# Performance work log

Hardware: AMD Instinct MI355X
Metric: run time of the kernel (lower is better)

## Reference

```python
import jax, jax.numpy as jnp
import numpy as np

IN_DIMS = [3, 16, 16]
OUT_DIMS = [16, 16, 3]
GRID_SIZE = 8
SPLINE_ORDER = 3
GRID_RANGE = (-1.0, 1.0)
K = GRID_SIZE + SPLINE_ORDER  # number of B-spline basis functions = 11

# extended knot grid, identical for every feature (as in standard KAN layers)
_h = (GRID_RANGE[1] - GRID_RANGE[0]) / GRID_SIZE
GRID_NP = np.arange(-SPLINE_ORDER, GRID_SIZE + SPLINE_ORDER + 1, dtype=np.float32) * _h + GRID_RANGE[0]

# per-layer parameter slice boundaries: [coef, univariate_weight, residual_weight] per layer
_sizes = [0]
for di, do in zip(IN_DIMS, OUT_DIMS):
    _sizes.extend([di * do * K, di * do, di * do])
PARAM_IDX = np.cumsum(_sizes)
KAN_PARAMS_NUM = int(PARAM_IDX[-1])  # 4576


def bspline_basis(x, grid):
    """Cox-de Boor recursion. x: [...,], grid: [G]. Returns [..., K]."""
    x = x[..., None]
    b = ((x >= grid[:-1]) & (x < grid[1:])).astype(x.dtype)
    for p in range(1, SPLINE_ORDER + 1):
        left = (x - grid[:-(p + 1)]) / (grid[p:-1] - grid[:-(p + 1)]) * b[..., :-1]
        right = (grid[p + 1:] - x) / (grid[p + 1:] - grid[1:-p]) * b[..., 1:]
        b = left + right
    return b  # [..., GRID_SIZE + SPLINE_ORDER]


def setup_inputs() -> dict:
    key = jax.random.key(0)
    k1, k2, k3, k4 = jax.random.split(key, 4)
    B, C, H, W = 8, 3, 224, 224
    x = jax.random.uniform(k1, (B, C, H, W), dtype=jnp.float32)  # in grid range
    features = jax.random.normal(k2, (B, 1000), dtype=jnp.float32)  # resnet18 output stand-in
    fc_w = jax.random.normal(k3, (KAN_PARAMS_NUM, 1000), dtype=jnp.float32) * 0.02
    fc_b = jax.random.normal(k4, (KAN_PARAMS_NUM,), dtype=jnp.float32) * 0.02
    return {"x": x, "features": features, "fc_w": fc_w, "fc_b": fc_b}


def reference(x, features, fc_w, fc_b):
    B, C, H, W = x.shape
    # hypernetwork head: per-sample flat KAN parameter vector [B, P]
    w = features @ fc_w.T + fc_b
    # image -> per-pixel tokens [B, T, C]
    y = jnp.transpose(x, (0, 2, 3, 1)).reshape(B, H * W, C)
    grid = jnp.asarray(GRID_NP, dtype=x.dtype)
    for n, (di, do) in enumerate(zip(IN_DIMS, OUT_DIMS)):
        i0, i1, i2, i3 = PARAM_IDX[3 * n: 3 * n + 4]
        coef = w[:, i0:i1].reshape(B, di, do, K)       # spline coefficients
        uw = w[:, i1:i2].reshape(B, di, do)            # univariate (spline) weight
        rw = w[:, i2:i3].reshape(B, di, do)            # residual (silu) weight
        basis = bspline_basis(y, grid)                 # [B, T, di, K]
        spline = jnp.einsum('btik,biok->bto', basis, coef * uw[..., None])
        base = jnp.einsum('bti,bio->bto', jax.nn.silu(y), rw)
        y = spline + base                              # [B, T, do]
    out = y.reshape(B, H, W, -1)
    return jnp.transpose(out, (0, 3, 1, 2))
```

## Files before the change

### kernel.cpp

```cpp
#include <hip/hip_runtime.h>

#define HW   50176
#define NPAR 4576

typedef _Float16 half8 __attribute__((ext_vector_type(8)));
typedef __fp16 fp16x2 __attribute__((ext_vector_type(2)));
typedef __attribute__((ext_vector_type(4))) float f32x4;
typedef __attribute__((ext_vector_type(4))) int int4v;

__device__ __forceinline__ unsigned short f2h(float f) {
    union { _Float16 h; unsigned short u; } c; c.h = (_Float16)f; return c.u;
}
__device__ __forceinline__ float h2f(unsigned short u) {
    union { _Float16 h; unsigned short u; } c; c.u = u; return (float)c.h;
}
__device__ __forceinline__ int pkrtz(float lo, float hi) {
    union { fp16x2 h; int i; } c;
    c.h = __builtin_amdgcn_cvt_pkrtz(lo, hi);
    return c.i;
}

__global__ __launch_bounds__(256) void gemm_w(const float* __restrict__ feats,
                                              const float* __restrict__ fcw,
                                              const float* __restrict__ fcb,
                                              float* __restrict__ wout) {
    __shared__ float red[4][64][4];
    int tid = threadIdx.x, lane = tid & 63, wave = tid >> 6;
    int nn = lane & 15, quad = lane >> 4;
    int n = blockIdx.x * 16 + nn;
    const float* brow = fcw + (size_t)n * 1000;
    const float* arow = feats + nn * 1000;

    f32x4 acc = {0.f, 0.f, 0.f, 0.f};
#pragma unroll 4
    for (int s8 = 0; s8 < 8; s8++) {
        int kb = (wave * 8 + s8) * 32 + quad * 8;
        float4 a0 = {0,0,0,0}, a1 = {0,0,0,0}, b0 = {0,0,0,0}, b1 = {0,0,0,0};
        if (kb < 1000) {
            b0 = *(const float4*)(brow + kb);
            b1 = *(const float4*)(brow + kb + 4);
            if (nn < 8) {
                a0 = *(const float4*)(arow + kb);
                a1 = *(const float4*)(arow + kb + 4);
            }
        }
        float af[8] = {a0.x, a0.y, a0.z, a0.w, a1.x, a1.y, a1.z, a1.w};
        float bf[8] = {b0.x, b0.y, b0.z, b0.w, b1.x, b1.y, b1.z, b1.w};
        half8 ah, al, bh;
#pragma unroll
        for (int j = 0; j < 8; j++) {
            ah[j] = (_Float16)af[j];
            al[j] = (_Float16)(af[j] - (float)ah[j]);
            bh[j] = (_Float16)bf[j];
        }
        acc = __builtin_amdgcn_mfma_f32_16x16x32_f16(ah, bh, acc, 0, 0, 0);
        acc = __builtin_amdgcn_mfma_f32_16x16x32_f16(al, bh, acc, 0, 0, 0);
    }
#pragma unroll
    for (int r = 0; r < 4; r++) red[wave][lane][r] = acc[r];
    __syncthreads();
    if (wave == 0 && quad < 2) {
        float bias = fcb[n];
#pragma unroll
        for (int r = 0; r < 4; r++) {
            float v = red[0][lane][r] + red[1][lane][r]
                    + red[2][lane][r] + red[3][lane][r];
            wout[(size_t)(quad * 4 + r) * NPAR + n] = v + bias;
        }
    }
}

__global__ __launch_bounds__(256) void pack_b(const float* __restrict__ w,
                                              unsigned int* __restrict__ bt) {
    int idx = blockIdx.x * 256 + threadIdx.x;
    if (idx >= 8 * 4608) return;
    int b = idx / 4608, r = idx - b * 4608;
    int ks = r >> 8, ln = (r >> 2) & 63, dq = r & 3;
    int q = ln >> 4, n = ln & 15;
    int lay, s;
    if (ks < 2)       { lay = 0; s = ks; }
    else if (ks < 10) { lay = 1; s = ks - 2; }
    else              { lay = 2; s = ks - 10; }
    int i = 2 * s + (q >> 1);
    const float* wb = w + b * NPAR;
    int cb, ub, rb2, nd, ni;
    if (lay == 0)      { cb = 0;    ub = 528;  rb2 = 576;  nd = 16; ni = 3;  }
    else if (lay == 1) { cb = 624;  ub = 3440; rb2 = 3696; nd = 16; ni = 16; }
    else               { cb = 3952; ub = 4480; rb2 = 4528; nd = 3;  ni = 16; }
    unsigned int pk = 0;
    if (i < ni && n < nd) {
        float uwv = wb[ub + i * nd + n];
        float rwv = wb[rb2 + i * nd + n];
        unsigned short rh = f2h(rwv);
        float rl = rwv - h2f(rh);
#pragma unroll
        for (int h = 0; h < 2; h++) {
            int rk = (q & 1) * 8 + dq * 2 + h;
            float v = 0.f;
            if (rk < 11)       v = wb[cb + (i * nd + n) * 11 + rk] * uwv;
            else if (rk < 13)  v = rwv;
            else if (rk == 13) v = rl;
            pk |= ((unsigned int)f2h(v)) << (16 * h);
        }
    }
    bt[idx] = pk;
}

__device__ __forceinline__ void compose_row(int4v& lo, int4v& hi, float y) {
    float t  = (y + 1.75f) * 4.0f;
    float ft = floorf(t);
    ft = fminf(fmaxf(ft, -8.0f), 24.0f);
    float u = t - ft;
    u = fminf(fmaxf(u, -8.0f), 8.0f);
    float u2 = u * u, u3 = u2 * u, om = 1.0f - u;
    float b0 = (1.0f / 6.0f) * om * om * om;
    float b3 = (1.0f / 6.0f) * u3;
    float b1 = 0.5f * u3 - u2 + (2.0f / 3.0f);
    float b2 = 1.0f - b0 - b1 - b3;

    int jt3 = (int)ft - 3;
    float z0 = ((unsigned)jt3 <= 10u)       ? b0 : 0.f;
    float z1 = ((unsigned)(jt3 + 1) <= 10u) ? b1 : 0.f;
    float z2 = ((unsigned)(jt3 + 2) <= 10u) ? b2 : 0.f;
    float z3 = ((unsigned)(jt3 + 3) <= 10u) ? b3 : 0.f;

    bool odd = (jt3 & 1) != 0;
    int I0 = pkrtz(odd ? 0.f : z0, odd ? z0 : z1);
    int I1 = pkrtz(odd ? z1 : z2, odd ? z2 : z3);
    int I2 = pkrtz(odd ? z3 : 0.f, 0.f);
    int m = jt3 >> 1;

    int d[6];
#pragma unroll
    for (int k = 0; k < 6; k++)
        d[k] = (k == m) ? I0 : (k == m + 1) ? I1 : (k == m + 2) ? I2 : 0;

    float sil = y * __builtin_amdgcn_rcpf(1.0f + __expf(-y));
    unsigned short sh = f2h(sil);
    float sl = sil - h2f(sh);

    lo[0] = d[0]; lo[1] = d[1]; lo[2] = d[2]; lo[3] = d[3];
    hi[0] = d[4];
    hi[1] = (d[5] & 0xFFFF) | ((int)((unsigned int)sh << 16));
    hi[2] = pkrtz(sl, sil);
    hi[3] = 0;
}

#define ASTR  20
#define YSTR  18
#define YBOFF (64 * ASTR)

__global__ __launch_bounds__(64) void kan_mfma(const float* __restrict__ x,
                                               const unsigned int* __restrict__ bt,
                                               float* __restrict__ out) {
    __shared__ __align__(16) int lds[YBOFF + 64 * YSTR];
    const int lane = threadIdx.x;
    const int quad = lane >> 4, nn = lane & 15;
    const int b = blockIdx.x / 784;
    const int px0 = (blockIdx.x - b * 784) * 64;
    const unsigned int* btb = bt + b * 4608;
    float* ybf = (float*)&lds[YBOFF];

    int4v* rowE = (int4v*)&lds[ASTR * lane];
    int4v* rowO = rowE + 2;
    const int aob = ASTR * nn + 4 * quad;

    const float* xg = x + (size_t)b * 3 * HW + px0 + lane;
    float xv0 = xg[0], xv1 = xg[HW], xv2 = xg[2 * HW];

    f32x4 acc[4];

    auto kstep2 = [&](int ks, float y0, float y1, bool doOdd) {
        union { half8 h; int4v v; } bf;
        bf.v = *(const int4v*)(btb + ks * 256 + lane * 4);
        int4v lo, hi;
        compose_row(lo, hi, y0);
        rowE[0] = lo; rowE[1] = hi;
        if (doOdd) {
            compose_row(lo, hi, y1);
            rowO[0] = lo; rowO[1] = hi;
        }
        asm volatile("s_waitcnt lgkmcnt(0)" ::: "memory");
#pragma unroll
        for (int mt = 0; mt < 4; mt++) {
            union { half8 h; int4v v; } af;
            af.v = *(int4v*)&lds[aob + mt * (16 * ASTR)];
            acc[mt] = __builtin_amdgcn_mfma_f32_16x16x32_f16(af.h, bf.h, acc[mt], 0, 0, 0);
        }
    };

#pragma unroll
    for (int mt = 0; mt < 4; mt++) acc[mt] = (f32x4){0.f, 0.f, 0.f, 0.f};
    kstep2(0, xv0, xv1, true);
    asm volatile("" ::: "memory");
    kstep2(1, xv2, 0.f, false);
#pragma unroll
    for (int mt = 0; mt < 4; mt++)
#pragma unroll
        for (int r = 0; r < 4; r++)
            ybf[(mt * 16 + quad * 4 + r) * YSTR + nn] = acc[mt][r];
    asm volatile("s_waitcnt lgkmcnt(0)" ::: "memory");

    {
        float yv[16];
#pragma unroll
        for (int j = 0; j < 8; j++) {
            float2 p = *(const float2*)&ybf[lane * YSTR + 2 * j];
            yv[2 * j] = p.x; yv[2 * j + 1] = p.y;
        }
#pragma unroll
        for (int mt = 0; mt < 4; mt++) acc[mt] = (f32x4){0.f, 0.f, 0.f, 0.f};
#pragma unroll 1
        for (int s = 0; s < 8; s++) {
            asm volatile("" ::: "memory");
            kstep2(2 + s, yv[2 * s], yv[2 * s + 1], true);
        }
    }
#pragma unroll
    for (int mt = 0; mt < 4; mt++)
#pragma unroll
        for (int r = 0; r < 4; r++)
            ybf[(mt * 16 + quad * 4 + r) * YSTR + nn] = acc[mt][r];
    asm volatile("s_waitcnt lgkmcnt(0)" ::: "memory");

    {
        float yv[16];
#pragma unroll
        for (int j = 0; j < 8; j++) {
            float2 p = *(const float2*)&ybf[lane * YSTR + 2 * j];
            yv[2 * j] = p.x; yv[2 * j + 1] = p.y;
        }
#pragma unroll
        for (int mt = 0; mt < 4; mt++) acc[mt] = (f32x4){0.f, 0.f, 0.f, 0.f};
#pragma unroll 1
        for (int s = 0; s < 8; s++) {
            asm volatile("" ::: "memory");
            kstep2(10 + s, yv[2 * s], yv[2 * s + 1], true);
        }
    }

    if (nn < 3) {
#pragma unroll
        for (int mt = 0; mt < 4; mt++)
#pragma unroll
            for (int r = 0; r < 4; r++)
                ybf[(mt * 16 + quad * 4 + r) * YSTR + nn] = acc[mt][r];
    }
    asm volatile("s_waitcnt lgkmcnt(0)" ::: "memory");
    float c0 = ybf[lane * YSTR + 0];
    float c1 = ybf[lane * YSTR + 1];
    float c2 = ybf[lane * YSTR + 2];
    float* ob = out + (size_t)b * 3 * HW + px0 + lane;
    ob[0]      = c0;
    ob[HW]     = c1;
    ob[2 * HW] = c2;
}

extern "C" void kernel_launch(void* const* d_in, const int* in_sizes, int n_in,
                              void* d_out, int out_size, void* d_ws, size_t ws_size,
                              hipStream_t stream) {
    const float* x     = (const float*)d_in[0];
    const float* feats = (const float*)d_in[1];
    const float* fcw   = (const float*)d_in[2];
    const float* fcb   = (const float*)d_in[3];
    float* outp = (float*)d_out;
    float* wbuf = (float*)d_ws;
    unsigned int* btens = (unsigned int*)d_ws + 36608;

    hipLaunchKernelGGL(gemm_w, dim3(286), dim3(256), 0, stream,
                       feats, fcw, fcb, wbuf);
    hipLaunchKernelGGL(pack_b, dim3(144), dim3(256), 0, stream,
                       wbuf, btens);
    hipLaunchKernelGGL(kan_mfma, dim3(8 * 784), dim3(64), 0, stream,
                       x, btens, outp);
}
```

Baseline: 119.1 us.

## Swap MFMA operand roles so basis is built in registers, drop LDS staging

The KAN MFMA kernel now processes 16 pixels per wave with the packed weights as the A operand and the per-pixel spline basis as the B operand, built directly in registers. This removes the LDS staging of basis rows, the LDS round-trip for intermediate layer outputs (replaced by cross-lane shuffles), and the waitcnt barriers. Blocks grow to 4 waves of 256 threads. In exchange each wave handles fewer pixels per weight fetch, so the weight tile is reloaded more often, and only a quarter of the lanes store output.

```diff
diff --git a/kernel.cpp b/kernel.cpp
--- a/kernel.cpp
+++ b/kernel.cpp
@@ -106,154 +106,99 @@
     bt[idx] = pk;
 }
 
-__device__ __forceinline__ void compose_row(int4v& lo, int4v& hi, float y) {
-    float t  = (y + 1.75f) * 4.0f;
-    float ft = floorf(t);
-    ft = fminf(fmaxf(ft, -8.0f), 24.0f);
-    float u = t - ft;
-    u = fminf(fmaxf(u, -8.0f), 8.0f);
-    float u2 = u * u, u3 = u2 * u, om = 1.0f - u;
-    float b0 = (1.0f / 6.0f) * om * om * om;
-    float b3 = (1.0f / 6.0f) * u3;
-    float b1 = 0.5f * u3 - u2 + (2.0f / 3.0f);
-    float b2 = 1.0f - b0 - b1 - b3;
-
-    int jt3 = (int)ft - 3;
-    float z0 = ((unsigned)jt3 <= 10u)       ? b0 : 0.f;
-    float z1 = ((unsigned)(jt3 + 1) <= 10u) ? b1 : 0.f;
-    float z2 = ((unsigned)(jt3 + 2) <= 10u) ? b2 : 0.f;
-    float z3 = ((unsigned)(jt3 + 3) <= 10u) ? b3 : 0.f;
-
-    bool odd = (jt3 & 1) != 0;
-    int I0 = pkrtz(odd ? 0.f : z0, odd ? z0 : z1);
-    int I1 = pkrtz(odd ? z1 : z2, odd ? z2 : z3);
-    int I2 = pkrtz(odd ? z3 : 0.f, 0.f);
-    int m = jt3 >> 1;
-
-    int d[6];
-#pragma unroll
-    for (int k = 0; k < 6; k++)
-        d[k] = (k == m) ? I0 : (k == m + 1) ? I1 : (k == m + 2) ? I2 : 0;
-
-    float sil = y * __builtin_amdgcn_rcpf(1.0f + __expf(-y));
-    unsigned short sh = f2h(sil);
-    float sl = sil - h2f(sh);
-
-    lo[0] = d[0]; lo[1] = d[1]; lo[2] = d[2]; lo[3] = d[3];
-    hi[0] = d[4];
-    hi[1] = (d[5] & 0xFFFF) | ((int)((unsigned int)sh << 16));
-    hi[2] = pkrtz(sl, sil);
-    hi[3] = 0;
-}
-
-#define ASTR  20
-#define YSTR  18
-#define YBOFF (64 * ASTR)
-
-__global__ __launch_bounds__(64) void kan_mfma(const float* __restrict__ x,
-                                               const unsigned int* __restrict__ bt,
-                                               float* __restrict__ out) {
-    __shared__ __align__(16) int lds[YBOFF + 64 * YSTR];
-    const int lane = threadIdx.x;
+__global__ __launch_bounds__(256) void kan_mfma(const float* __restrict__ x,
+                                                const unsigned int* __restrict__ bt,
+                                                float* __restrict__ out) {
+    const int tid  = threadIdx.x;
+    const int lane = tid & 63, wv = tid >> 6;
     const int quad = lane >> 4, nn = lane & 15;
-    const int b = blockIdx.x / 784;
-    const int px0 = (blockIdx.x - b * 784) * 64;
+    const int g  = quad & 1;
+    const int hi = quad >> 1;
+    const int g4 = g * 4;
+    const int gtile = blockIdx.x * 4 + wv;
+    const int b = gtile / 3136;
+    const int px0 = (gtile - b * 3136) * 16;
     const unsigned int* btb = bt + b * 4608;
-    float* ybf = (float*)&lds[YBOFF];
-
-    int4v* rowE = (int4v*)&lds[ASTR * lane];
-    int4v* rowO = rowE + 2;
-    const int aob = ASTR * nn + 4 * quad;
-
-    const float* xg = x + (size_t)b * 3 * HW + px0 + lane;
-    float xv0 = xg[0], xv1 = xg[HW], xv2 = xg[2 * HW];
-
-    f32x4 acc[4];
-
-    auto kstep2 = [&](int ks, float y0, float y1, bool doOdd) {
-        union { half8 h; int4v v; } bf;
-        bf.v = *(const int4v*)(btb + ks * 256 + lane * 4);
-        int4v lo, hi;
-        compose_row(lo, hi, y0);
-        rowE[0] = lo; rowE[1] = hi;
-        if (doOdd) {
-            compose_row(lo, hi, y1);
-            rowO[0] = lo; rowO[1] = hi;
-        }
-        asm volatile("s_waitcnt lgkmcnt(0)" ::: "memory");
-#pragma unroll
-        for (int mt = 0; mt < 4; mt++) {
-            union { half8 h; int4v v; } af;
-            af.v = *(int4v*)&lds[aob + mt * (16 * ASTR)];
-            acc[mt] = __builtin_amdgcn_mfma_f32_16x16x32_f16(af.h, bf.h, acc[mt], 0, 0, 0);
-        }
+
+    const float* xb = x + (size_t)b * 3 * HW + px0 + nn;
+    float xv0 = xb[0], xv1 = xb[HW], xv2 = xb[2 * HW];
+
+    auto composeB = [&](float y) -> int4v {
+        float t  = (y + 1.75f) * 4.0f;
+        float ft = floorf(t);
+        ft = fminf(fmaxf(ft, -8.0f), 24.0f);
+        float u = t - ft;
+        u = fminf(fmaxf(u, -8.0f), 8.0f);
+        float u2 = u * u, u3 = u2 * u, om = 1.0f - u;
+        float b0 = (1.0f / 6.0f) * om * om * om;
+        float b3 = (1.0f / 6.0f) * u3;
+        float b1 = 0.5f * u3 - u2 + (2.0f / 3.0f);
+        float b2 = 1.0f - b0 - b1 - b3;
+        int jt3 = (int)ft - 3;
+        float z0 = ((unsigned)jt3       <= 10u) ? b0 : 0.f;
+        float z1 = ((unsigned)(jt3 + 1) <= 10u) ? b1 : 0.f;
+        float z2 = ((unsigned)(jt3 + 2) <= 10u) ? b2 : 0.f;
+        float z3 = ((unsigned)(jt3 + 3) <= 10u) ? b3 : 0.f;
+        bool odd = (jt3 & 1) != 0;
+        int I0 = pkrtz(odd ? 0.f : z0, odd ? z0 : z1);
+        int I1 = pkrtz(odd ? z1 : z2, odd ? z2 : z3);
+        int I2 = pkrtz(odd ? z3 : 0.f, 0.f);
+        int mrel = (jt3 >> 1) - g4;
+        int4v d;
+#pragma unroll
+        for (int k = 0; k < 4; k++) {
+            int e = k - mrel;
+            d[k] = (e == 0) ? I0 : (e == 1) ? I1 : (e == 2) ? I2 : 0;
+        }
+        float sil = y * __builtin_amdgcn_rcpf(1.0f + __expf(-y));
+        unsigned short sh = f2h(sil);
+        float sl = sil - h2f(sh);
+        d[1] |= g ? (int)((unsigned int)sh << 16) : 0;
+        d[2] |= g ? pkrtz(sl, sil) : 0;
+        return d;
     };
 
-#pragma unroll
-    for (int mt = 0; mt < 4; mt++) acc[mt] = (f32x4){0.f, 0.f, 0.f, 0.f};
-    kstep2(0, xv0, xv1, true);
-    asm volatile("" ::: "memory");
-    kstep2(1, xv2, 0.f, false);
-#pragma unroll
-    for (int mt = 0; mt < 4; mt++)
-#pragma unroll
-        for (int r = 0; r < 4; r++)
-            ybf[(mt * 16 + quad * 4 + r) * YSTR + nn] = acc[mt][r];
-    asm volatile("s_waitcnt lgkmcnt(0)" ::: "memory");
-
+    auto kstep = [&](int ks, float y, f32x4& a) {
+        union { half8 h; int4v v; } af, bf;
+        af.v = *(const int4v*)(btb + ks * 256 + lane * 4);
+        bf.v = composeB(y);
+        a = __builtin_amdgcn_mfma_f32_16x16x32_f16(af.h, bf.h, a, 0, 0, 0);
+    };
+
+    f32x4 a1 = {0.f, 0.f, 0.f, 0.f};
+    kstep(0, hi ? xv1 : xv0, a1);
+    kstep(1, xv2, a1);
+
+    f32x4 a2 = {0.f, 0.f, 0.f, 0.f};
     {
-        float yv[16];
-#pragma unroll
-        for (int j = 0; j < 8; j++) {
-            float2 p = *(const float2*)&ybf[lane * YSTR + 2 * j];
-            yv[2 * j] = p.x; yv[2 * j + 1] = p.y;
-        }
-#pragma unroll
-        for (int mt = 0; mt < 4; mt++) acc[mt] = (f32x4){0.f, 0.f, 0.f, 0.f};
-#pragma unroll 1
+        float p0 = a1[0], p1 = a1[1], p2 = a1[2], p3 = a1[3];
+#pragma unroll
         for (int s = 0; s < 8; s++) {
-            asm volatile("" ::: "memory");
-            kstep2(2 + s, yv[2 * s], yv[2 * s + 1], true);
-        }
-    }
-#pragma unroll
-    for (int mt = 0; mt < 4; mt++)
-#pragma unroll
-        for (int r = 0; r < 4; r++)
-            ybf[(mt * 16 + quad * 4 + r) * YSTR + nn] = acc[mt][r];
-    asm volatile("s_waitcnt lgkmcnt(0)" ::: "memory");
-
+            int srcl = (s >> 1) * 16 + nn;
+            float yc0 = __shfl((s & 1) ? p2 : p0, srcl, 64);
+            float yc1 = __shfl((s & 1) ? p3 : p1, srcl, 64);
+            kstep(2 + s, hi ? yc1 : yc0, a2);
+        }
+    }
+
+    f32x4 a3 = {0.f, 0.f, 0.f, 0.f};
     {
-        float yv[16];
-#pragma unroll
-        for (int j = 0; j < 8; j++) {
-            float2 p = *(const float2*)&ybf[lane * YSTR + 2 * j];
-            yv[2 * j] = p.x; yv[2 * j + 1] = p.y;
-        }
-#pragma unroll
-        for (int mt = 0; mt < 4; mt++) acc[mt] = (f32x4){0.f, 0.f, 0.f, 0.f};
-#pragma unroll 1
+        float p0 = a2[0], p1 = a2[1], p2 = a2[2], p3 = a2[3];
+#pragma unroll
         for (int s = 0; s < 8; s++) {
-            asm volatile("" ::: "memory");
-            kstep2(10 + s, yv[2 * s], yv[2 * s + 1], true);
-        }
-    }
-
-    if (nn < 3) {
-#pragma unroll
-        for (int mt = 0; mt < 4; mt++)
-#pragma unroll
-            for (int r = 0; r < 4; r++)
-                ybf[(mt * 16 + quad * 4 + r) * YSTR + nn] = acc[mt][r];
-    }
-    asm volatile("s_waitcnt lgkmcnt(0)" ::: "memory");
-    float c0 = ybf[lane * YSTR + 0];
-    float c1 = ybf[lane * YSTR + 1];
-    float c2 = ybf[lane * YSTR + 2];
-    float* ob = out + (size_t)b * 3 * HW + px0 + lane;
-    ob[0]      = c0;
-    ob[HW]     = c1;
-    ob[2 * HW] = c2;
+            int srcl = (s >> 1) * 16 + nn;
+            float yc0 = __shfl((s & 1) ? p2 : p0, srcl, 64);
+            float yc1 = __shfl((s & 1) ? p3 : p1, srcl, 64);
+            kstep(10 + s, hi ? yc1 : yc0, a3);
+        }
+    }
+
+    if (quad == 0) {
+        float* ob = out + (size_t)b * 3 * HW + px0 + nn;
+        ob[0]      = a3[0];
+        ob[HW]     = a3[1];
+        ob[2 * HW] = a3[2];
+    }
 }
 
 extern "C" void kernel_launch(void* const* d_in, const int* in_sizes, int n_in,
@@ -271,6 +216,6 @@
                        feats, fcw, fcb, wbuf);
     hipLaunchKernelGGL(pack_b, dim3(144), dim3(256), 0, stream,
                        wbuf, btens);
-    hipLaunchKernelGGL(kan_mfma, dim3(8 * 784), dim3(64), 0, stream,
+    hipLaunchKernelGGL(kan_mfma, dim3(6272), dim3(256), 0, stream,
                        x, btens, outp);
 }
```

Result: slower. 144.4 us (+21.2%).
